# Kernel optimization log

Hardware: AMD Instinct MI355X
Metric: run time of the kernel (lower is better)

## Reference

```python
import jax, jax.numpy as jnp
import numpy as np

H = 256  # hidden_channels
N_USERS = 100000
N_MOVIES = 50000
N_EDGES = 500000


def setup_inputs() -> dict:
    key = jax.random.key(0)
    k1, k2, k3, k4, k5, k6, k7 = jax.random.split(key, 7)
    user_emb = jax.random.normal(k1, (N_USERS, H), dtype=jnp.float32)
    movie_emb = jax.random.normal(k2, (N_MOVIES, H), dtype=jnp.float32)
    edge_label_index = jax.random.randint(k3, (2, N_EDGES), 0, N_MOVIES, dtype=jnp.int64)
    # Linear(2H, H) and Linear(H, 1) params, torch default init scale
    s1 = 1.0 / np.sqrt(2 * H)
    s2 = 1.0 / np.sqrt(H)
    W1 = jax.random.uniform(k4, (2 * H, H), dtype=jnp.float32, minval=-s1, maxval=s1)
    b1 = jax.random.uniform(k5, (H,), dtype=jnp.float32, minval=-s1, maxval=s1)
    W2 = jax.random.uniform(k6, (H, 1), dtype=jnp.float32, minval=-s2, maxval=s2)
    b2 = jax.random.uniform(k7, (1,), dtype=jnp.float32, minval=-s2, maxval=s2)
    return {"user_emb": user_emb, "movie_emb": movie_emb,
            "edge_label_index": edge_label_index,
            "W1": W1, "b1": b1, "W2": W2, "b2": b2}


def reference(user_emb, movie_emb, edge_label_index, W1, b1, W2, b2):
    u = user_emb[edge_label_index[0]]    # [E, H]
    m = movie_emb[edge_label_index[1]]   # [E, H]
    x = jnp.concatenate([u, m], axis=-1)  # [E, 2H]
    x = jax.nn.relu(x @ W1 + b1)          # [E, H]
    return x @ W2 + b2                    # [E, 1]
```

## Files before the change

kernel.cpp:

```cpp
#include <hip/hip_runtime.h>
#include <hip/hip_bf16.h>

typedef __attribute__((ext_vector_type(8))) short v8s;
typedef __attribute__((ext_vector_type(4))) float v4f;

constexpr int H  = 256;
constexpr int K2 = 512;
constexpr int XS = 72;
constexpr int WS = 72;

__device__ inline unsigned short f2bf(float f) {
    unsigned int u = __builtin_bit_cast(unsigned int, f);
    u += 0x7FFFu + ((u >> 16) & 1u);
    return (unsigned short)(u >> 16);
}
__device__ inline float bf2f(unsigned short s) {
    return __builtin_bit_cast(float, (unsigned int)s << 16);
}

#define SB() __builtin_amdgcn_sched_barrier(0)
#define VMW(N) do { asm volatile("s_waitcnt vmcnt(" #N ")" ::: "memory"); SB(); } while (0)

__global__ void w1_transpose_kernel(const float* __restrict__ w1,
                                    unsigned short* __restrict__ w1t,
                                    unsigned char* __restrict__ flags,
                                    const int nflags) {
    __shared__ float tile[32][33];
    const int bk = blockIdx.x;
    const int bn = blockIdx.y;
    const int tx = threadIdx.x & 31;
    const int ty8 = threadIdx.x >> 5;
    if (flags && bk == 0 && bn == 0) {
        for (int i = threadIdx.x; i < nflags; i += 256) flags[i] = 0;
    }
#pragma unroll
    for (int i = 0; i < 4; ++i) {
        int ty = i * 8 + ty8;
        tile[ty][tx] = w1[(size_t)(bk * 32 + ty) * H + bn * 32 + tx];
    }
    __syncthreads();
#pragma unroll
    for (int i = 0; i < 4; ++i) {
        int ty = i * 8 + ty8;
        w1t[(size_t)(bn * 32 + ty) * K2 + bk * 32 + tx] = f2bf(tile[tx][ty]);
    }
}

__global__ void flag_fill_kernel(const int* __restrict__ eli,
                                 unsigned char* __restrict__ fu,
                                 unsigned char* __restrict__ fm,
                                 const int E, const int nu, const int nm) {
    const long stride = (long)blockDim.x * gridDim.x;
    for (long e = threadIdx.x + (long)blockIdx.x * blockDim.x; e < E; e += stride) {
        int u = eli[e];
        int m = eli[(long)E + e];
        u = u < 0 ? 0 : (u >= nu ? nu - 1 : u);
        m = m < 0 ? 0 : (m >= nm ? nm - 1 : m);
        fu[u >> 6] = 1;
        fm[m >> 6] = 1;
    }
}

__global__ __launch_bounds__(512, 2) void emb_gemm_persist_kernel(
    const float* __restrict__ user_emb,
    const float* __restrict__ movie_emb,
    const unsigned short* __restrict__ w1t,
    const float* __restrict__ b1,
    unsigned short* __restrict__ P,
    unsigned short* __restrict__ Q,
    const int n_users, const int n_movies,
    const unsigned char* __restrict__ fu,
    const unsigned char* __restrict__ fm)
{
    __shared__ __align__(16) char Xs[2][64][1024];

    const int bid   = blockIdx.x;
    const int nside = (int)(gridDim.x >> 1);
    const int isMovie = bid & 1;
    const int base  = bid >> 1;

    const float* emb = isMovie ? movie_emb : user_emb;
    unsigned short* outp = isMovie ? Q : P;
    const int M    = isMovie ? n_movies : n_users;
    const int kofs = isMovie ? 256 : 0;
    const int nch  = (M + 63) >> 6;
    const unsigned char* flags = isMovie ? fm : fu;

    const int t    = threadIdx.x;
    const int wave = t >> 6;
    const int lane = t & 63;
    const int wm   = wave >> 2;
    const int wn   = wave & 3;
    const int quad = lane >> 4;
    const int l16  = lane & 15;

    unsigned long long mk;
    {
        int c = base + lane * nside;
        bool a = (c < nch) && (flags[c] != 0);
        mk = __ballot(a);
    }
    const int nact = (int)__popcll(mk);
    if (nact == 0) return;

    unsigned long long cur = mk, pf = mk;
    auto nextc = [&](unsigned long long& m) -> int {
        int p = (int)__builtin_ctzll(m);
        m &= m - 1;
        return base + p * nside;
    };

    v8s B[4][4][2];
    {
        const unsigned short* wb = w1t + (size_t)(wn * 64 + l16) * K2 + kofs + quad * 8;
#pragma unroll
        for (int nt = 0; nt < 4; ++nt)
#pragma unroll
            for (int kt = 0; kt < 4; ++kt)
#pragma unroll
                for (int ks = 0; ks < 2; ++ks)
                    B[nt][kt][ks] = *(const v8s*)(wb + (size_t)nt * 16 * K2 + kt * 64 + ks * 32);
    }
    float bv[4];
#pragma unroll
    for (int nt = 0; nt < 4; ++nt)
        bv[nt] = isMovie ? 0.f : b1[wn * 64 + nt * 16 + l16];
    SB();

    auto KEEPB = [&]() {
#pragma unroll
        for (int nt = 0; nt < 4; ++nt)
#pragma unroll
            for (int kt = 0; kt < 4; ++kt)
#pragma unroll
                for (int ks = 0; ks < 2; ++ks)
                    asm volatile("" : "+v"(B[nt][kt][ks]));
    };

    auto STAGE = [&](int c, int b) {
#pragma unroll
        for (int i = 0; i < 8; ++i) {
            const int rl = wave * 8 + i;
            long r = (long)c * 64 + rl;
            if (r >= M) r = M - 1;
            const char* src = (const char*)(emb + (size_t)r * H) + ((lane * 16) ^ (i << 4));
            __builtin_amdgcn_global_load_lds(
                (const __attribute__((address_space(1))) unsigned int*)src,
                (__attribute__((address_space(3))) unsigned int*)&Xs[b][rl][0],
                16, 0, 0);
        }
        SB();
    };

    STAGE(nextc(pf), 0);
    if (nact > 1) STAGE(nextc(pf), 1);

    for (int j = 0; j < nact; ++j) {
        const int cb = j & 1;
        const long m0 = (long)nextc(cur) * 64;

        KEEPB();

        if (j == 0) { if (nact > 1) VMW(8); else VMW(0); }
        else        { if (j + 1 < nact) VMW(40); else VMW(32); }
        __builtin_amdgcn_s_barrier(); SB();

        v4f acc[2][4];
#pragma unroll
        for (int mt = 0; mt < 2; ++mt)
#pragma unroll
            for (int nt = 0; nt < 4; ++nt)
                acc[mt][nt] = (v4f){0.f, 0.f, 0.f, 0.f};

        const char* xb = &Xs[cb][0][0];
#pragma unroll
        for (int kk = 0; kk < 8; ++kk) {
            v8s af[2];
#pragma unroll
            for (int mt = 0; mt < 2; ++mt) {
                const int row = wm * 32 + mt * 16 + l16;
                const int sw  = (row & 7) << 4;
                const char* pr = xb + row * 1024;
                v4f f0 = *(const v4f*)(pr + ((kk * 128 + quad * 32) ^ sw));
                v4f f1 = *(const v4f*)(pr + ((kk * 128 + quad * 32 + 16) ^ sw));
                v8s a;
#pragma unroll
                for (int q2 = 0; q2 < 4; ++q2) {
                    a[q2]     = (short)f2bf(f0[q2]);
                    a[4 + q2] = (short)f2bf(f1[q2]);
                }
                af[mt] = a;
            }
#pragma unroll
            for (int mt = 0; mt < 2; ++mt)
#pragma unroll
                for (int nt = 0; nt < 4; ++nt)
                    acc[mt][nt] = __builtin_amdgcn_mfma_f32_16x16x32_bf16(
                        af[mt], B[nt][kk >> 1][kk & 1], acc[mt][nt], 0, 0, 0);
        }

#pragma unroll
        for (int mt = 0; mt < 2; ++mt)
#pragma unroll
            for (int j4 = 0; j4 < 4; ++j4) {
                const long m = m0 + wm * 32 + mt * 16 + quad * 4 + j4;
#pragma unroll
                for (int nt = 0; nt < 4; ++nt)
                    outp[(size_t)m * H + wn * 64 + nt * 16 + l16] =
                        f2bf(acc[mt][nt][j4] + bv[nt]);
            }
        SB();
        __builtin_amdgcn_s_barrier(); SB();
        if (j + 2 < nact) STAGE(nextc(pf), cb);
    }
}

__global__ __launch_bounds__(256, 8) void edge_score_kernel(
    const unsigned short* __restrict__ P,
    const unsigned short* __restrict__ Q,
    const int* __restrict__ eli,
    const float* __restrict__ w2,
    const float* __restrict__ b2,
    float* __restrict__ out,
    const int E, const int n_users, const int n_movies, const long e0)
{
    const int t   = threadIdx.x;
    const int hw  = t >> 5;
    const int l32 = t & 31;

    float w2v[8];
    {
        v4f a = *(const v4f*)(w2 + l32 * 8);
        v4f b = *(const v4f*)(w2 + l32 * 8 + 4);
#pragma unroll
        for (int i = 0; i < 4; ++i) { w2v[i] = a[i]; w2v[4 + i] = b[i]; }
    }
    const float b2v = b2[0];
    const long base = e0 + (long)blockIdx.x * 64;

    int us[8], ms[8];
#pragma unroll
    for (int i = 0; i < 8; ++i) {
        long e = base + i * 8 + hw;
        long ec = (e < E) ? e : 0;
        int u = eli[ec];
        int m = eli[(long)E + ec];
        us[i] = u < 0 ? 0 : (u >= n_users  ? n_users  - 1 : u);
        ms[i] = m < 0 ? 0 : (m >= n_movies ? n_movies - 1 : m);
    }

    v8s pv = *(const v8s*)(P + (size_t)us[0] * H + l32 * 8);
    v8s qv = *(const v8s*)(Q + (size_t)ms[0] * H + l32 * 8);

#pragma unroll
    for (int i = 0; i < 8; ++i) {
        v8s pn, qn;
        if (i < 7) {
            pn = *(const v8s*)(P + (size_t)us[i + 1] * H + l32 * 8);
            qn = *(const v8s*)(Q + (size_t)ms[i + 1] * H + l32 * 8);
        }
        float s = 0.f;
#pragma unroll
        for (int j = 0; j < 8; ++j) {
            float h = bf2f((unsigned short)pv[j]) + bf2f((unsigned short)qv[j]);
            h = h > 0.f ? h : 0.f;
            s += h * w2v[j];
        }
        s += __shfl_xor(s, 1, 64);
        s += __shfl_xor(s, 2, 64);
        s += __shfl_xor(s, 4, 64);
        s += __shfl_xor(s, 8, 64);
        s += __shfl_xor(s, 16, 64);
        long e = base + i * 8 + hw;
        if (l32 == 0 && e < E) out[e] = s + b2v;
        pv = pn; qv = qn;
    }
}

constexpr int BMF = 64;
__global__ __launch_bounds__(512, 4) void edge_decoder_kernel(
    const float* __restrict__ user_emb, const float* __restrict__ movie_emb,
    const int* __restrict__ eli, const unsigned short* __restrict__ w1t,
    const float* __restrict__ b1, const float* __restrict__ w2,
    const float* __restrict__ b2, float* __restrict__ out,
    const int E, const int n_users, const int n_movies)
{
    __shared__ unsigned short Xs[BMF * XS];
    __shared__ unsigned short Wts[H * WS];
    __shared__ float red[4][BMF];
    const int t = threadIdx.x, wave = t >> 6, lane = t & 63;
    const int wm = wave >> 2, wn = wave & 3, quad = lane >> 4, l16 = lane & 15;
    const long e0 = (long)blockIdx.x * BMF;
    const int xr = t >> 3, xc = t & 7;
    long eg = e0 + xr; if (eg >= E) eg = 0;
    int iu = eli[eg], im = eli[(long)E + eg];
    iu = iu < 0 ? 0 : (iu >= n_users ? n_users - 1 : iu);
    im = im < 0 ? 0 : (im >= n_movies ? n_movies - 1 : im);
    const float* urow = user_emb + (size_t)iu * H;
    const float* mrow = movie_emb + (size_t)im * H;
    const int wr = t >> 3, wc8 = t & 7;
    const unsigned short* wbase = w1t + (size_t)wr * K2 + wc8 * 8;
    v4f acc[2][4];
#pragma unroll
    for (int mt = 0; mt < 2; ++mt)
#pragma unroll
        for (int nt = 0; nt < 4; ++nt) acc[mt][nt] = (v4f){0.f,0.f,0.f,0.f};
    v4f xq0 = *(const v4f*)(urow + xc * 8);
    v4f xq1 = *(const v4f*)(urow + xc * 8 + 4);
    v8s wq[4];
#pragma unroll
    for (int j = 0; j < 4; ++j) wq[j] = *(const v8s*)(wbase + (size_t)j * 64 * K2);
    for (int kt = 0; kt < 8; ++kt) {
        __syncthreads();
        { v8s xv;
#pragma unroll
          for (int i = 0; i < 4; ++i) xv[i] = (short)f2bf(xq0[i]);
#pragma unroll
          for (int i = 0; i < 4; ++i) xv[4+i] = (short)f2bf(xq1[i]);
          *(v8s*)(Xs + xr * XS + xc * 8) = xv; }
#pragma unroll
        for (int j = 0; j < 4; ++j) *(v8s*)(Wts + (j * 64 + wr) * WS + wc8 * 8) = wq[j];
        if (kt < 7) {
            const int kn = kt + 1, koff = (kn * 64) & 255;
            const float* src = ((kn < 4) ? urow : mrow) + koff + xc * 8;
            xq0 = *(const v4f*)(src); xq1 = *(const v4f*)(src + 4);
#pragma unroll
            for (int j = 0; j < 4; ++j) wq[j] = *(const v8s*)(wbase + (size_t)j * 64 * K2 + kn * 64);
        }
        __syncthreads();
#pragma unroll
        for (int ks = 0; ks < 2; ++ks) {
            v8s af[2], bf[4];
#pragma unroll
            for (int mt = 0; mt < 2; ++mt)
                af[mt] = *(const v8s*)(Xs + (wm * 32 + mt * 16 + l16) * XS + ks * 32 + quad * 8);
#pragma unroll
            for (int nt = 0; nt < 4; ++nt)
                bf[nt] = *(const v8s*)(Wts + (wn * 64 + nt * 16 + l16) * WS + ks * 32 + quad * 8);
#pragma unroll
            for (int mt = 0; mt < 2; ++mt)
#pragma unroll
                for (int nt = 0; nt < 4; ++nt)
                    acc[mt][nt] = __builtin_amdgcn_mfma_f32_16x16x32_bf16(af[mt], bf[nt], acc[mt][nt], 0, 0, 0);
        }
    }
    float b1v[4], w2v[4];
#pragma unroll
    for (int nt = 0; nt < 4; ++nt) {
        int n = wn * 64 + nt * 16 + l16;
        b1v[nt] = b1[n]; w2v[nt] = w2[n];
    }
    const float b2v = b2[0];
#pragma unroll
    for (int mt = 0; mt < 2; ++mt) {
        float s[4] = {0.f,0.f,0.f,0.f};
#pragma unroll
        for (int nt = 0; nt < 4; ++nt)
#pragma unroll
            for (int j = 0; j < 4; ++j) {
                float h = acc[mt][nt][j] + b1v[nt];
                h = h > 0.f ? h : 0.f;
                s[j] += h * w2v[nt];
            }
#pragma unroll
        for (int j = 0; j < 4; ++j) {
            float v = s[j];
            v += __shfl_xor(v, 1, 64); v += __shfl_xor(v, 2, 64);
            v += __shfl_xor(v, 4, 64); v += __shfl_xor(v, 8, 64);
            if (l16 == 0) red[wn][wm * 32 + mt * 16 + quad * 4 + j] = v;
        }
    }
    __syncthreads();
    if (t < BMF) {
        long e = e0 + t;
        if (e < E) out[e] = red[0][t] + red[1][t] + red[2][t] + red[3][t] + b2v;
    }
}

extern "C" void kernel_launch(void* const* d_in, const int* in_sizes, int n_in,
                              void* d_out, int out_size, void* d_ws, size_t ws_size,
                              hipStream_t stream) {
    const float* user_emb  = (const float*)d_in[0];
    const float* movie_emb = (const float*)d_in[1];
    const int*   eli       = (const int*)d_in[2];
    const float* w1        = (const float*)d_in[3];
    const float* b1        = (const float*)d_in[4];
    const float* w2        = (const float*)d_in[5];
    const float* b2        = (const float*)d_in[6];
    float*       out       = (float*)d_out;

    const int E        = out_size;
    const int n_users  = in_sizes[0] / H;
    const int n_movies = in_sizes[1] / H;

    unsigned short* w1t = (unsigned short*)d_ws;
    const size_t w1t_bytes = (size_t)K2 * H * 2;
    const size_t p_bytes   = (size_t)(n_users  + 64) * H * 2;
    const size_t q_bytes   = (size_t)(n_movies + 64) * H * 2;

    const int nbu = (n_users  + 63) / 64;
    const int nbm = (n_movies + 63) / 64;
    const size_t flag_bytes = (size_t)nbu + (size_t)nbm;

    if (ws_size >= w1t_bytes + p_bytes + q_bytes + flag_bytes &&
        nbu <= 64 * 128 && nbm <= 64 * 128) {
        unsigned short* P = (unsigned short*)((char*)d_ws + w1t_bytes);
        unsigned short* Q = (unsigned short*)((char*)d_ws + w1t_bytes + p_bytes);
        unsigned char*  fu = (unsigned char*)((char*)d_ws + w1t_bytes + p_bytes + q_bytes);
        unsigned char*  fm = fu + nbu;

        w1_transpose_kernel<<<dim3(16, 8), 256, 0, stream>>>(w1, w1t, fu, nbu + nbm);
        if (E > 0)
            flag_fill_kernel<<<512, 256, 0, stream>>>(eli, fu, fm, E, n_users, n_movies);
        emb_gemm_persist_kernel<<<256, 512, 0, stream>>>(
            user_emb, movie_emb, w1t, b1, P, Q, n_users, n_movies, fu, fm);
        if (E > 0) {
            long Eh = ((long)(E / 2) + 63) & ~63L;
            if (Eh > E) Eh = E;
            if (Eh > 0)
                edge_score_kernel<<<(int)(Eh / 64), 256, 0, stream>>>(
                    P, Q, eli, w2, b2, out, E, n_users, n_movies, 0);
            if (E - Eh > 0)
                edge_score_kernel<<<(int)((E - Eh + 63) / 64), 256, 0, stream>>>(
                    P, Q, eli, w2, b2, out, E, n_users, n_movies, Eh);
        }
    } else {
        w1_transpose_kernel<<<dim3(16, 8), 256, 0, stream>>>(w1, w1t, nullptr, 0);
        if (E > 0)
            edge_decoder_kernel<<<(E + BMF - 1) / BMF, 512, 0, stream>>>(
                user_emb, movie_emb, eli, w1t, b1, w2, b2, out, E, n_users, n_movies);
    }
}
```

Baseline: 272.4 us.

## Load GEMM A-operand straight from global into registers instead of LDS staging

Drops the double-buffered LDS staging (global_load_lds plus barriers) in the persistent embedding GEMM. Each lane now loads its fp32 A fragment straight from global memory into registers, with a two-deep register prefetch that crosses into the next chunk. The fp32-to-bf16 conversion now uses the packed v_cvt_pk_bf16_f32 instruction instead of manual rounding. This removes LDS traffic and block barriers, but global loads become less coalesced (32-byte pieces per lane) and load latency is hidden only by the register prefetch.

```diff
diff --git a/kernel.cpp b/kernel.cpp
--- a/kernel.cpp
+++ b/kernel.cpp
@@ -17,9 +17,6 @@
 __device__ inline float bf2f(unsigned short s) {
     return __builtin_bit_cast(float, (unsigned int)s << 16);
 }
-
-#define SB() __builtin_amdgcn_sched_barrier(0)
-#define VMW(N) do { asm volatile("s_waitcnt vmcnt(" #N ")" ::: "memory"); SB(); } while (0)
 
 __global__ void w1_transpose_kernel(const float* __restrict__ w1,
                                     unsigned short* __restrict__ w1t,
@@ -72,8 +69,6 @@
     const unsigned char* __restrict__ fu,
     const unsigned char* __restrict__ fm)
 {
-    __shared__ __align__(16) char Xs[2][64][1024];
-
     const int bid   = blockIdx.x;
     const int nside = (int)(gridDim.x >> 1);
     const int isMovie = bid & 1;
@@ -96,14 +91,14 @@
 
     unsigned long long mk;
     {
-        int c = base + lane * nside;
-        bool a = (c < nch) && (flags[c] != 0);
+        int c0 = base + lane * nside;
+        bool a = (c0 < nch) && (flags[c0] != 0);
         mk = __ballot(a);
     }
     const int nact = (int)__popcll(mk);
     if (nact == 0) return;
 
-    unsigned long long cur = mk, pf = mk;
+    unsigned long long cur = mk;
     auto nextc = [&](unsigned long long& m) -> int {
         int p = (int)__builtin_ctzll(m);
         m &= m - 1;
@@ -125,7 +120,6 @@
 #pragma unroll
     for (int nt = 0; nt < 4; ++nt)
         bv[nt] = isMovie ? 0.f : b1[wn * 64 + nt * 16 + l16];
-    SB();
 
     auto KEEPB = [&]() {
 #pragma unroll
@@ -137,33 +131,52 @@
                     asm volatile("" : "+v"(B[nt][kt][ks]));
     };
 
-    auto STAGE = [&](int c, int b) {
-#pragma unroll
-        for (int i = 0; i < 8; ++i) {
-            const int rl = wave * 8 + i;
-            long r = (long)c * 64 + rl;
+    const float* pA[2];
+    const float* pN[2];
+    auto SETP = [&](const float** p, int c) {
+#pragma unroll
+        for (int mt = 0; mt < 2; ++mt) {
+            long r = (long)c * 64 + wm * 32 + mt * 16 + l16;
             if (r >= M) r = M - 1;
-            const char* src = (const char*)(emb + (size_t)r * H) + ((lane * 16) ^ (i << 4));
-            __builtin_amdgcn_global_load_lds(
-                (const __attribute__((address_space(1))) unsigned int*)src,
-                (__attribute__((address_space(3))) unsigned int*)&Xs[b][rl][0],
-                16, 0, 0);
-        }
-        SB();
+            p[mt] = emb + (size_t)r * H;
+        }
     };
 
-    STAGE(nextc(pf), 0);
-    if (nact > 1) STAGE(nextc(pf), 1);
+    v4f xf[2][2][2];
+    auto LOADA = [&](int b, const float** p, int kk) {
+#pragma unroll
+        for (int mt = 0; mt < 2; ++mt) {
+            const float* s = p[mt] + kk * 32 + quad * 8;
+            xf[b][mt][0] = *(const v4f*)(s);
+            xf[b][mt][1] = *(const v4f*)(s + 4);
+        }
+    };
+    auto CONV = [&](v8s* af, int b) {
+#pragma unroll
+        for (int mt = 0; mt < 2; ++mt) {
+            union { v8s s; unsigned int w[4]; } u;
+            asm("v_cvt_pk_bf16_f32 %0, %1, %2"
+                : "=v"(u.w[0]) : "v"(xf[b][mt][0][0]), "v"(xf[b][mt][0][1]));
+            asm("v_cvt_pk_bf16_f32 %0, %1, %2"
+                : "=v"(u.w[1]) : "v"(xf[b][mt][0][2]), "v"(xf[b][mt][0][3]));
+            asm("v_cvt_pk_bf16_f32 %0, %1, %2"
+                : "=v"(u.w[2]) : "v"(xf[b][mt][1][0]), "v"(xf[b][mt][1][1]));
+            asm("v_cvt_pk_bf16_f32 %0, %1, %2"
+                : "=v"(u.w[3]) : "v"(xf[b][mt][1][2]), "v"(xf[b][mt][1][3]));
+            af[mt] = u.s;
+        }
+    };
+
+    int c = nextc(cur);
+    SETP(pA, c);
+    LOADA(0, pA, 0);
+    LOADA(1, pA, 1);
 
     for (int j = 0; j < nact; ++j) {
-        const int cb = j & 1;
-        const long m0 = (long)nextc(cur) * 64;
-
         KEEPB();
-
-        if (j == 0) { if (nact > 1) VMW(8); else VMW(0); }
-        else        { if (j + 1 < nact) VMW(40); else VMW(32); }
-        __builtin_amdgcn_s_barrier(); SB();
+        const long m0 = (long)c * 64;
+        const int cn = cur ? (base + (int)__builtin_ctzll(cur) * nside) : c;
+        SETP(pN, cn);
 
         v4f acc[2][4];
 #pragma unroll
@@ -172,25 +185,12 @@
             for (int nt = 0; nt < 4; ++nt)
                 acc[mt][nt] = (v4f){0.f, 0.f, 0.f, 0.f};
 
-        const char* xb = &Xs[cb][0][0];
 #pragma unroll
         for (int kk = 0; kk < 8; ++kk) {
             v8s af[2];
-#pragma unroll
-            for (int mt = 0; mt < 2; ++mt) {
-                const int row = wm * 32 + mt * 16 + l16;
-                const int sw  = (row & 7) << 4;
-                const char* pr = xb + row * 1024;
-                v4f f0 = *(const v4f*)(pr + ((kk * 128 + quad * 32) ^ sw));
-                v4f f1 = *(const v4f*)(pr + ((kk * 128 + quad * 32 + 16) ^ sw));
-                v8s a;
-#pragma unroll
-                for (int q2 = 0; q2 < 4; ++q2) {
-                    a[q2]     = (short)f2bf(f0[q2]);
-                    a[4 + q2] = (short)f2bf(f1[q2]);
-                }
-                af[mt] = a;
-            }
+            CONV(af, kk & 1);
+            if (kk < 6) LOADA(kk & 1, pA, kk + 2);
+            else        LOADA(kk & 1, pN, kk - 6);
 #pragma unroll
             for (int mt = 0; mt < 2; ++mt)
 #pragma unroll
@@ -209,9 +209,10 @@
                     outp[(size_t)m * H + wn * 64 + nt * 16 + l16] =
                         f2bf(acc[mt][nt][j4] + bv[nt]);
             }
-        SB();
-        __builtin_amdgcn_s_barrier(); SB();
-        if (j + 2 < nact) STAGE(nextc(pf), cb);
+
+        pA[0] = pN[0]; pA[1] = pN[1];
+        c = cn;
+        if (j + 1 < nact) cur &= cur - 1;
     }
 }
 
```

New measurement: 306.9 us. 1.13x slower.
